# Kernel optimization log

Measured on AMD Instinct MI355X. Metric: run time of the kernel, lower is better.

## Reference

```python
import jax, jax.numpy as jnp
import numpy as np

STRIDE = 1
PAD_INIT = 0


def _im2col(x, k, stride, padding):
    # torch.nn.functional.unfold equivalent: channel order (C, kh, kw), row-major spatial
    patches = jax.lax.conv_general_dilated_patches(
        x, (k, k), (stride, stride), [(padding, padding), (padding, padding)])
    # patches: (N, C*k*k, h_out, w_out)
    N, d, ho, wo = patches.shape
    # match torch code: view(N, d, L').permute(1,2,0).reshape(d, L'*N)
    X_col = patches.reshape(N, d, ho * wo).transpose(1, 2, 0).reshape(d, ho * wo * N)
    return X_col, ho, wo


def setup_inputs() -> dict:
    key = jax.random.key(0)
    k1, k2 = jax.random.split(key)
    x = jax.random.normal(k1, (32, 128, 28, 28), dtype=jnp.float32)
    W = jax.random.normal(k2, (128, 128, 3, 3), dtype=jnp.float32)
    return {"x": x, "W": W}


def reference(x, W):
    F_, C, kh, kw = W.shape
    N, _, H, _ = x.shape
    # 'full' conv output size per the module's formula
    h_out = (H - 1) * STRIDE - 2 * PAD_INIT + (kh - 1) + 1
    pad = ((h_out - 1) * STRIDE + kh - H) // 2
    X_col, ho, wo = _im2col(x, kh, STRIDE, pad)          # (d, L), d=C*k*k, L=ho*wo*N
    W_col = W.reshape(F_, -1)                            # (F, d)
    # intended quadratic 'adder' decomposition: out[f,l] = -0.5*||W_f - X_l||^2
    # = W_f . X_l - 0.5*||W_f||^2 - 0.5*||X_l||^2  (fused GEMM form, no (F,d,L) blowup)
    out = (W_col @ X_col
           - 0.5 * jnp.sum(W_col * W_col, axis=1)[:, None]
           - 0.5 * jnp.sum(X_col * X_col, axis=0)[None, :])  # (F, L)
    out = out.reshape(F_, ho, wo, N).transpose(3, 0, 1, 2)   # (N, F, ho, wo)
    return out
```

## Files before the change

### kernel.cpp

```cpp
#include <hip/hip_runtime.h>
#include <hip/hip_bf16.h>
#include <stdint.h>


#define N_IMG 32
#define C_IN 128
#define H_IN 28
#define HP 32
#define HO 30
#define P_SP 900
#define F_OUT 128
#define K_TOT 1152

#define BLT 60
#define TPI 15
#define NBLK (N_IMG*TPI)
#define NSTEP 18

typedef __attribute__((ext_vector_type(8))) short bf16x8;
typedef __attribute__((ext_vector_type(4))) unsigned short u16x4;
typedef __attribute__((ext_vector_type(8))) unsigned short u16x8;
typedef __attribute__((ext_vector_type(4))) float f32x4;

__device__ __forceinline__ unsigned short f2bf(float f) {
  union { float f; unsigned u; } t; t.f = f;
  unsigned r = t.u + 0x7fffu + ((t.u >> 16) & 1u);
  return (unsigned short)(r >> 16);
}

__global__ void prep_w_kernel(const float* __restrict__ W,
                              unsigned short* __restrict__ Wbf,
                              float* __restrict__ wnorm) {
  int f = blockIdx.x;
  const float* Wf = W + f * K_TOT;
  float part = 0.f;
  for (int k = threadIdx.x; k < K_TOT; k += 256) {
    float v = Wf[k];
    part += v * v;
    int ch = k / 9, rr = k - ch * 9;
    Wbf[f * K_TOT + rr * 128 + ch] = f2bf(v);
  }
  __shared__ float red[256];
  red[threadIdx.x] = part;
  __syncthreads();
  for (int st = 128; st > 0; st >>= 1) {
    if (threadIdx.x < st) red[threadIdx.x] += red[threadIdx.x + st];
    __syncthreads();
  }
  if (threadIdx.x == 0) wnorm[f] = 0.5f * red[0];
}

__global__ __launch_bounds__(256, 2) void adder_fused_kernel(
    const float* __restrict__ x,
    const unsigned short* __restrict__ Wbf,
    const float* __restrict__ wnorm,
    float* __restrict__ out) {
  __shared__ unsigned short xfoot[128 * 130];
  __shared__ unsigned short A_lds[2][64 * 128];
  __shared__ float pixsum_s[128];
  __shared__ float xn_s[64];
  __shared__ float wn_s[F_OUT];

  int tid = threadIdx.x, lane = tid & 63, wid = tid >> 6;
  int bid0 = blockIdx.x;
  int bid = (bid0 & 7) * (NBLK / 8) + (bid0 >> 3);
  int n = bid / TPI, timg = bid - n * TPI;
  int i0 = timg * 2, p0 = timg * BLT;

  char* XF = (char*)xfoot;
  char* A0 = (char*)&A_lds[0][0];
  char* A1 = (char*)&A_lds[1][0];
  const char* WbfB = (const char*)Wbf;

  int kb = ((lane & 7) * 16) ^ ((lane >> 3) << 4);
  int a_goff[4];
#pragma unroll
  for (int a = 0; a < 4; a++) {
    int q = a * 4 + wid;
    int rowf = q * 8 + (lane >> 3);
    a_goff[a] = rowf * (K_TOT * 2) + kb;
  }
  int a_loff = wid * 1024 + lane * 16;

  auto STAGE = [&](int t, char* AB) {
    int off = t * 128;
#pragma unroll
    for (int a = 0; a < 4; a++)
      __builtin_amdgcn_global_load_lds(
          (const __attribute__((address_space(1))) void*)(WbfB + a_goff[a] + off),
          (__attribute__((address_space(3))) void*)(AB + a * 4096 + a_loff), 16, 0, 0);
  };

  if (tid < F_OUT) wn_s[tid] = wnorm[tid];
  STAGE(0, A0);
  STAGE(1, A1);

  for (int u = tid; u < 896; u += 256) {
    int cq = u / 28, rem = u - cq * 28;
    int r = rem / 7, w4 = rem - r * 7;
    int c = cq * 4;
    int hr = i0 - 2 + r;
    float vv[4][4];
    if (hr >= 0 && hr < H_IN) {
#pragma unroll
      for (int q = 0; q < 4; q++) {
        float4 t4 = *(const float4*)(x + (((n * C_IN + c + q) * H_IN + hr) * H_IN + w4 * 4));
        vv[q][0] = t4.x; vv[q][1] = t4.y; vv[q][2] = t4.z; vv[q][3] = t4.w;
      }
    } else {
#pragma unroll
      for (int q = 0; q < 4; q++)
#pragma unroll
        for (int e = 0; e < 4; e++) vv[q][e] = 0.f;
    }
#pragma unroll
    for (int e = 0; e < 4; e++) {
      int wp = w4 * 4 + e + 2;
      int pix = r * 32 + wp;
      u16x4 o;
#pragma unroll
      for (int q = 0; q < 4; q++) o[q] = f2bf(vv[q][e]);
      *(u16x4*)(XF + pix * 256 + ((c * 2) ^ ((pix & 15) << 4))) = o;
    }
  }
  {
    int r = tid >> 6, wi = (tid >> 4) & 3, slot = tid & 15;
    int wp = (wi < 2) ? wi : 28 + wi;
    int pix = r * 32 + wp;
    u16x8 z;
#pragma unroll
    for (int q = 0; q < 8; q++) z[q] = 0;
    *(u16x8*)(XF + pix * 256 + ((slot * 16) ^ ((pix & 15) << 4))) = z;
  }
  __syncthreads();

  {
    int pix = tid >> 1, ch = tid & 1;
    float ssum = 0.f;
#pragma unroll
    for (int q = 0; q < 8; q++) {
      u16x8 v8 = *(const u16x8*)(XF + pix * 256 + (((ch * 128) + q * 16) ^ ((pix & 15) << 4)));
#pragma unroll
      for (int e = 0; e < 8; e++) {
        union { unsigned u; float f; } cv; cv.u = ((unsigned)v8[e]) << 16;
        ssum += cv.f * cv.f;
      }
    }
    ssum += __shfl_xor(ssum, 1);
    if (!ch) pixsum_s[pix] = ssum;
  }
  __syncthreads();
  if (tid < BLT) {
    int il = tid / HO, j = tid - il * HO;
    float a9 = 0.f;
#pragma unroll
    for (int dh = 0; dh < 3; dh++)
#pragma unroll
      for (int dw = 0; dw < 3; dw++)
        a9 += pixsum_s[(il + dh) * 32 + (j + dw)];
    xn_s[tid] = 0.5f * a9;
  }
  __syncthreads();

  f32x4 acc[4][2];
#pragma unroll
  for (int mi = 0; mi < 4; mi++)
#pragma unroll
    for (int ni = 0; ni < 2; ni++)
      acc[mi][ni] = (f32x4){0.f, 0.f, 0.f, 0.f};

  int wr = wid >> 1, wc = wid & 1;
  int pix0[2];
#pragma unroll
  for (int ni = 0; ni < 2; ni++) {
    int cc = wc * 32 + ni * 16 + (lane & 15);
    if (cc > BLT - 1) cc = BLT - 1;
    int il = cc / HO, j = cc - il * HO;
    pix0[ni] = il * 32 + j;
  }
  int kfrag = (lane >> 4) * 16;

#pragma unroll 2
  for (int t = 0; t < NSTEP; t++) {
    char* ABc = (t & 1) ? A1 : A0;
    int rr = t >> 1, half = t & 1;
    int dh = rr / 3, dw = rr - 3 * dh;
    int pofs = dh * 32 + dw;
    int bbase = half * 128;
#pragma unroll
    for (int kc = 0; kc < 2; kc++) {
      bf16x8 af[4], bfv[2];
#pragma unroll
      for (int mi = 0; mi < 4; mi++) {
        int rowf = wr * 64 + mi * 16 + (lane & 15);
        af[mi] = *(const bf16x8*)(ABc + rowf * 128 + ((kc * 64 + kfrag) ^ ((rowf & 7) << 4)));
      }
#pragma unroll
      for (int ni = 0; ni < 2; ni++) {
        int pix = pix0[ni] + pofs;
        bfv[ni] = *(const bf16x8*)(XF + pix * 256 + ((bbase + kc * 64 + kfrag) ^ ((pix & 15) << 4)));
      }
      __builtin_amdgcn_s_setprio(1);
#pragma unroll
      for (int mi = 0; mi < 4; mi++)
#pragma unroll
        for (int ni = 0; ni < 2; ni++)
          acc[mi][ni] = __builtin_amdgcn_mfma_f32_16x16x32_bf16(
              af[mi], bfv[ni], acc[mi][ni], 0, 0, 0);
      __builtin_amdgcn_s_setprio(0);
    }
    __builtin_amdgcn_s_barrier();
    if (t + 2 < NSTEP) {
      STAGE(t + 2, ABc);
      asm volatile("s_waitcnt vmcnt(4)" ::: "memory");
      __builtin_amdgcn_s_barrier();
    } else if (t + 2 == NSTEP) {
      asm volatile("s_waitcnt vmcnt(0)" ::: "memory");
      __builtin_amdgcn_s_barrier();
    }
  }
  __syncthreads();

  float* Cst = (float*)xfoot;
  int colc = lane & 15, kg = lane >> 4;
#pragma unroll
  for (int mi = 0; mi < 4; mi++) {
    int f0 = wr * 64 + mi * 16 + kg * 4;
#pragma unroll
    for (int ni = 0; ni < 2; ni++) {
      int cc = wc * 32 + ni * 16 + colc;
#pragma unroll
      for (int r = 0; r < 4; r++)
        Cst[(f0 + r) * 65 + cc] = acc[mi][ni][r];
    }
  }
  __syncthreads();
  {
    int col = tid & 63, fq = tid >> 6;
    if (col < BLT) {
      float xn = xn_s[col];
      float* ob = out + (size_t)n * (F_OUT * P_SP) + p0 + col;
#pragma unroll
      for (int q = 0; q < 32; q++) {
        int f = fq * 32 + q;
        __builtin_nontemporal_store(Cst[f * 65 + col] - wn_s[f] - xn, ob + f * P_SP);
      }
    }
  }
}

extern "C" void kernel_launch(void* const* d_in, const int* in_sizes, int n_in,
                              void* d_out, int out_size, void* d_ws, size_t ws_size,
                              hipStream_t stream) {
  const float* x = (const float*)d_in[0];
  const float* W = (const float*)d_in[1];
  float* out = (float*)d_out;

  char* ws = (char*)d_ws;
  unsigned short* Wbf = (unsigned short*)(ws);
  float* wnorm = (float*)(ws + 294912);

  prep_w_kernel<<<F_OUT, 256, 0, stream>>>(W, Wbf, wnorm);
  adder_fused_kernel<<<NBLK, 256, 0, stream>>>(x, Wbf, wnorm, out);
}
```

Before: 26.87 us.

## Pre-swizzle weights into MFMA fragment order and load A directly from global

```diff
diff --git a/kernel.cpp b/kernel.cpp
--- a/kernel.cpp
+++ b/kernel.cpp
@@ -29,34 +29,42 @@
 }
 
 __global__ void prep_w_kernel(const float* __restrict__ W,
-                              unsigned short* __restrict__ Wbf,
+                              unsigned short* __restrict__ Wfrag,
                               float* __restrict__ wnorm) {
   int f = blockIdx.x;
   const float* Wf = W + f * K_TOT;
+  int t = threadIdx.x;
   float part = 0.f;
-  for (int k = threadIdx.x; k < K_TOT; k += 256) {
-    float v = Wf[k];
-    part += v * v;
-    int ch = k / 9, rr = k - ch * 9;
-    Wbf[f * K_TOT + rr * 128 + ch] = f2bf(v);
+  if (t < 144) {
+    int rr = t / 16, rem = t & 15;
+    int ks = rem >> 2, kg = rem & 3;
+    u16x8 o;
+#pragma unroll
+    for (int e = 0; e < 8; e++) {
+      int ch = ks * 32 + kg * 8 + e;
+      float v = Wf[ch * 9 + rr];
+      part += v * v;
+      o[e] = f2bf(v);
+    }
+    int off = ((rr * 4 + ks) * 8 + (f >> 4)) * 512 + (kg * 16 + (f & 15)) * 8;
+    *(u16x8*)(&Wfrag[off]) = o;
   }
   __shared__ float red[256];
-  red[threadIdx.x] = part;
+  red[t] = part;
   __syncthreads();
   for (int st = 128; st > 0; st >>= 1) {
-    if (threadIdx.x < st) red[threadIdx.x] += red[threadIdx.x + st];
+    if (t < st) red[t] += red[t + st];
     __syncthreads();
   }
-  if (threadIdx.x == 0) wnorm[f] = 0.5f * red[0];
+  if (t == 0) wnorm[f] = 0.5f * red[0];
 }
 
 __global__ __launch_bounds__(256, 2) void adder_fused_kernel(
     const float* __restrict__ x,
-    const unsigned short* __restrict__ Wbf,
+    const unsigned short* __restrict__ Wfrag,
     const float* __restrict__ wnorm,
     float* __restrict__ out) {
   __shared__ unsigned short xfoot[128 * 130];
-  __shared__ unsigned short A_lds[2][64 * 128];
   __shared__ float pixsum_s[128];
   __shared__ float xn_s[64];
   __shared__ float wn_s[F_OUT];
@@ -68,32 +76,8 @@
   int i0 = timg * 2, p0 = timg * BLT;
 
   char* XF = (char*)xfoot;
-  char* A0 = (char*)&A_lds[0][0];
-  char* A1 = (char*)&A_lds[1][0];
-  const char* WbfB = (const char*)Wbf;
-
-  int kb = ((lane & 7) * 16) ^ ((lane >> 3) << 4);
-  int a_goff[4];
-#pragma unroll
-  for (int a = 0; a < 4; a++) {
-    int q = a * 4 + wid;
-    int rowf = q * 8 + (lane >> 3);
-    a_goff[a] = rowf * (K_TOT * 2) + kb;
-  }
-  int a_loff = wid * 1024 + lane * 16;
-
-  auto STAGE = [&](int t, char* AB) {
-    int off = t * 128;
-#pragma unroll
-    for (int a = 0; a < 4; a++)
-      __builtin_amdgcn_global_load_lds(
-          (const __attribute__((address_space(1))) void*)(WbfB + a_goff[a] + off),
-          (__attribute__((address_space(3))) void*)(AB + a * 4096 + a_loff), 16, 0, 0);
-  };
 
   if (tid < F_OUT) wn_s[tid] = wnorm[tid];
-  STAGE(0, A0);
-  STAGE(1, A1);
 
   for (int u = tid; u < 896; u += 256) {
     int cq = u / 28, rem = u - cq * 28;
@@ -170,35 +154,32 @@
       acc[mi][ni] = (f32x4){0.f, 0.f, 0.f, 0.f};
 
   int wr = wid >> 1, wc = wid & 1;
+  int colc = lane & 15, kg = lane >> 4;
+  int kfrag = kg * 16;
   int pix0[2];
 #pragma unroll
   for (int ni = 0; ni < 2; ni++) {
-    int cc = wc * 32 + ni * 16 + (lane & 15);
+    int cc = wc * 32 + ni * 16 + colc;
     if (cc > BLT - 1) cc = BLT - 1;
     int il = cc / HO, j = cc - il * HO;
     pix0[ni] = il * 32 + j;
   }
-  int kfrag = (lane >> 4) * 16;
-
-#pragma unroll 2
-  for (int t = 0; t < NSTEP; t++) {
-    char* ABc = (t & 1) ? A1 : A0;
-    int rr = t >> 1, half = t & 1;
-    int dh = rr / 3, dw = rr - 3 * dh;
-    int pofs = dh * 32 + dw;
-    int bbase = half * 128;
-#pragma unroll
-    for (int kc = 0; kc < 2; kc++) {
+  const char* Abase = (const char*)Wfrag + wr * 4096 + (size_t)lane * 16;
+
+#pragma unroll
+  for (int rr = 0; rr < 9; rr++) {
+    const int dh = rr / 3, dw = rr - 3 * dh;
+    const int pofs = dh * 32 + dw;
+#pragma unroll
+    for (int ks = 0; ks < 4; ks++) {
       bf16x8 af[4], bfv[2];
 #pragma unroll
-      for (int mi = 0; mi < 4; mi++) {
-        int rowf = wr * 64 + mi * 16 + (lane & 15);
-        af[mi] = *(const bf16x8*)(ABc + rowf * 128 + ((kc * 64 + kfrag) ^ ((rowf & 7) << 4)));
-      }
+      for (int mi = 0; mi < 4; mi++)
+        af[mi] = *(const bf16x8*)(Abase + ((rr * 4 + ks) * 8192 + mi * 1024));
 #pragma unroll
       for (int ni = 0; ni < 2; ni++) {
         int pix = pix0[ni] + pofs;
-        bfv[ni] = *(const bf16x8*)(XF + pix * 256 + ((bbase + kc * 64 + kfrag) ^ ((pix & 15) << 4)));
+        bfv[ni] = *(const bf16x8*)(XF + pix * 256 + ((ks * 64 + kfrag) ^ ((pix & 15) << 4)));
       }
       __builtin_amdgcn_s_setprio(1);
 #pragma unroll
@@ -209,20 +190,10 @@
               af[mi], bfv[ni], acc[mi][ni], 0, 0, 0);
       __builtin_amdgcn_s_setprio(0);
     }
-    __builtin_amdgcn_s_barrier();
-    if (t + 2 < NSTEP) {
-      STAGE(t + 2, ABc);
-      asm volatile("s_waitcnt vmcnt(4)" ::: "memory");
-      __builtin_amdgcn_s_barrier();
-    } else if (t + 2 == NSTEP) {
-      asm volatile("s_waitcnt vmcnt(0)" ::: "memory");
-      __builtin_amdgcn_s_barrier();
-    }
   }
   __syncthreads();
 
   float* Cst = (float*)xfoot;
-  int colc = lane & 15, kg = lane >> 4;
 #pragma unroll
   for (int mi = 0; mi < 4; mi++) {
     int f0 = wr * 64 + mi * 16 + kg * 4;
@@ -257,9 +228,9 @@
   float* out = (float*)d_out;
 
   char* ws = (char*)d_ws;
-  unsigned short* Wbf = (unsigned short*)(ws);
+  unsigned short* Wfrag = (unsigned short*)(ws);
   float* wnorm = (float*)(ws + 294912);
 
-  prep_w_kernel<<<F_OUT, 256, 0, stream>>>(W, Wbf, wnorm);
-  adder_fused_kernel<<<NBLK, 256, 0, stream>>>(x, Wbf, wnorm, out);
-}
+  prep_w_kernel<<<F_OUT, 256, 0, stream>>>(W, Wfrag, wnorm);
+  adder_fused_kernel<<<NBLK, 256, 0, stream>>>(x, Wfrag, wnorm, out);
+}
```

After: 28.08 us. 1.05x slower.

## Replace double-buffered async W staging with register-prefetched single buffer per tap

Applied to the files above, without the earlier changes.

```diff
diff --git a/kernel.cpp b/kernel.cpp
--- a/kernel.cpp
+++ b/kernel.cpp
@@ -15,7 +15,6 @@
 #define BLT 60
 #define TPI 15
 #define NBLK (N_IMG*TPI)
-#define NSTEP 18
 
 typedef __attribute__((ext_vector_type(8))) short bf16x8;
 typedef __attribute__((ext_vector_type(4))) unsigned short u16x4;
@@ -56,7 +55,7 @@
     const float* __restrict__ wnorm,
     float* __restrict__ out) {
   __shared__ unsigned short xfoot[128 * 130];
-  __shared__ unsigned short A_lds[2][64 * 128];
+  __shared__ unsigned short A_lds[128 * 128];
   __shared__ float pixsum_s[128];
   __shared__ float xn_s[64];
   __shared__ float wn_s[F_OUT];
@@ -68,32 +67,28 @@
   int i0 = timg * 2, p0 = timg * BLT;
 
   char* XF = (char*)xfoot;
-  char* A0 = (char*)&A_lds[0][0];
-  char* A1 = (char*)&A_lds[1][0];
+  char* AB = (char*)A_lds;
   const char* WbfB = (const char*)Wbf;
 
-  int kb = ((lane & 7) * 16) ^ ((lane >> 3) << 4);
-  int a_goff[4];
-#pragma unroll
-  for (int a = 0; a < 4; a++) {
-    int q = a * 4 + wid;
-    int rowf = q * 8 + (lane >> 3);
-    a_goff[a] = rowf * (K_TOT * 2) + kb;
-  }
-  int a_loff = wid * 1024 + lane * 16;
-
-  auto STAGE = [&](int t, char* AB) {
-    int off = t * 128;
-#pragma unroll
-    for (int a = 0; a < 4; a++)
+  {
+#pragma unroll
+    for (int a = 0; a < 8; a++) {
+      int q = a * 4 + wid;
+      int row = q * 4 + (lane >> 4);
+      int goff = row * (K_TOT * 2) + (((lane & 15) * 16) ^ ((row & 7) << 4));
       __builtin_amdgcn_global_load_lds(
-          (const __attribute__((address_space(1))) void*)(WbfB + a_goff[a] + off),
-          (__attribute__((address_space(3))) void*)(AB + a * 4096 + a_loff), 16, 0, 0);
-  };
-
+          (const __attribute__((address_space(1))) void*)(WbfB + goff),
+          (__attribute__((address_space(3))) void*)(AB + q * 1024 + lane * 16), 16, 0, 0);
+    }
+  }
   if (tid < F_OUT) wn_s[tid] = wnorm[tid];
-  STAGE(0, A0);
-  STAGE(1, A1);
+
+  int grs[8];
+#pragma unroll
+  for (int s = 0; s < 8; s++) {
+    int row = s * 16 + (tid >> 4);
+    grs[s] = row * (K_TOT * 2) + (((tid & 15) * 16) ^ ((row & 7) << 4));
+  }
 
   for (int u = tid; u < 896; u += 256) {
     int cq = u / 28, rem = u - cq * 28;
@@ -170,35 +165,43 @@
       acc[mi][ni] = (f32x4){0.f, 0.f, 0.f, 0.f};
 
   int wr = wid >> 1, wc = wid & 1;
+  int colc = lane & 15, kg = lane >> 4;
+  int kfrag = kg * 16;
   int pix0[2];
 #pragma unroll
   for (int ni = 0; ni < 2; ni++) {
-    int cc = wc * 32 + ni * 16 + (lane & 15);
+    int cc = wc * 32 + ni * 16 + colc;
     if (cc > BLT - 1) cc = BLT - 1;
     int il = cc / HO, j = cc - il * HO;
     pix0[ni] = il * 32 + j;
   }
-  int kfrag = (lane >> 4) * 16;
-
-#pragma unroll 2
-  for (int t = 0; t < NSTEP; t++) {
-    char* ABc = (t & 1) ? A1 : A0;
-    int rr = t >> 1, half = t & 1;
-    int dh = rr / 3, dw = rr - 3 * dh;
+  int arow[4], asw[4];
+#pragma unroll
+  for (int mi = 0; mi < 4; mi++) {
+    arow[mi] = (wr * 64 + mi * 16 + colc) * 256;
+    asw[mi] = ((wr * 64 + mi * 16 + colc) & 7) << 4;
+  }
+
+  u16x8 rs[8];
+  for (int t = 0; t < 9; t++) {
+    if (t + 1 < 9) {
+      int off = (t + 1) * 256;
+#pragma unroll
+      for (int s = 0; s < 8; s++)
+        rs[s] = *(const u16x8*)(WbfB + grs[s] + off);
+    }
+    int dh = t / 3, dw = t - 3 * dh;
     int pofs = dh * 32 + dw;
-    int bbase = half * 128;
-#pragma unroll
-    for (int kc = 0; kc < 2; kc++) {
+#pragma unroll
+    for (int kc = 0; kc < 4; kc++) {
       bf16x8 af[4], bfv[2];
 #pragma unroll
-      for (int mi = 0; mi < 4; mi++) {
-        int rowf = wr * 64 + mi * 16 + (lane & 15);
-        af[mi] = *(const bf16x8*)(ABc + rowf * 128 + ((kc * 64 + kfrag) ^ ((rowf & 7) << 4)));
-      }
+      for (int mi = 0; mi < 4; mi++)
+        af[mi] = *(const bf16x8*)(AB + arow[mi] + ((kc * 64 + kfrag) ^ asw[mi]));
 #pragma unroll
       for (int ni = 0; ni < 2; ni++) {
         int pix = pix0[ni] + pofs;
-        bfv[ni] = *(const bf16x8*)(XF + pix * 256 + ((bbase + kc * 64 + kfrag) ^ ((pix & 15) << 4)));
+        bfv[ni] = *(const bf16x8*)(XF + pix * 256 + ((kc * 64 + kfrag) ^ ((pix & 15) << 4)));
       }
       __builtin_amdgcn_s_setprio(1);
 #pragma unroll
@@ -209,20 +212,16 @@
               af[mi], bfv[ni], acc[mi][ni], 0, 0, 0);
       __builtin_amdgcn_s_setprio(0);
     }
-    __builtin_amdgcn_s_barrier();
-    if (t + 2 < NSTEP) {
-      STAGE(t + 2, ABc);
-      asm volatile("s_waitcnt vmcnt(4)" ::: "memory");
-      __builtin_amdgcn_s_barrier();
-    } else if (t + 2 == NSTEP) {
-      asm volatile("s_waitcnt vmcnt(0)" ::: "memory");
-      __builtin_amdgcn_s_barrier();
-    }
-  }
-  __syncthreads();
+    __syncthreads();
+    if (t + 1 < 9) {
+#pragma unroll
+      for (int s = 0; s < 8; s++)
+        *(u16x8*)(AB + s * 4096 + tid * 16) = rs[s];
+      __syncthreads();
+    }
+  }
 
   float* Cst = (float*)xfoot;
-  int colc = lane & 15, kg = lane >> 4;
 #pragma unroll
   for (int mi = 0; mi < 4; mi++) {
     int f0 = wr * 64 + mi * 16 + kg * 4;
```

Result: slower. 27.42 us (+2.1%).
